# Optimization experiments

Hardware: AMD Instinct MI355X
Metric: run time of the kernel (lower is better)

The kernel has to match this reference:

```python
import jax, jax.numpy as jnp
import numpy as np

D_MODEL = 1024
NUM_HEADS = 16
SEQ_LEN = 2048
HEAD_DIM = D_MODEL // NUM_HEADS


def _rope_thetas(seq_len, head_dim):
    # Standard RoPE angles: theta[s, j] = s * 10000^(-2j/d), j in [0, d/2)
    d_half = head_dim // 2
    pos = jnp.arange(seq_len, dtype=jnp.float32)
    freqs = 1.0 / jnp.power(10000.0, jnp.arange(0, head_dim, 2, dtype=jnp.float32) / head_dim)
    thetas = pos[:, None] * freqs[None, :]  # [S, d_half]
    return jnp.cos(thetas), jnp.sin(thetas)


def _apply_rope(x, cos, sin):
    # x: [B, H, S, D]; rotate consecutive pairs (x_{2i}, x_{2i+1}) by theta_i
    b, h, s, d = x.shape
    xp = x.reshape(b, h, s, d // 2, 2)
    x1, x2 = xp[..., 0], xp[..., 1]
    c = cos[None, None, :, :]
    sn = sin[None, None, :, :]
    o1 = x1 * c - x2 * sn
    o2 = x1 * sn + x2 * c
    return jnp.stack([o1, o2], axis=-1).reshape(b, h, s, d)


def setup_inputs() -> dict:
    key = jax.random.key(0)
    k_x, k_wqkv, k_bqkv, k_wo, k_bo = jax.random.split(key, 5)
    lim_qkv = 1.0 / np.sqrt(D_MODEL)
    x = jax.random.normal(k_x, (2, SEQ_LEN, D_MODEL), dtype=jnp.float32)
    w_qkv = jax.random.uniform(k_wqkv, (3 * D_MODEL, D_MODEL), jnp.float32, -lim_qkv, lim_qkv)
    b_qkv = jax.random.uniform(k_bqkv, (3 * D_MODEL,), jnp.float32, -lim_qkv, lim_qkv)
    w_out = jax.random.uniform(k_wo, (D_MODEL, D_MODEL), jnp.float32, -lim_qkv, lim_qkv)
    b_out = jax.random.uniform(k_bo, (D_MODEL,), jnp.float32, -lim_qkv, lim_qkv)
    return {"x": x, "w_qkv": w_qkv, "b_qkv": b_qkv, "w_out": w_out, "b_out": b_out}


def reference(x, w_qkv, b_qkv, w_out, b_out):
    B, S, D = x.shape
    H, Dh = NUM_HEADS, D // NUM_HEADS
    qkv = x @ w_qkv.T + b_qkv  # [B, S, 3D]
    q, k, v = jnp.split(qkv, 3, axis=-1)
    # [B, S, D] -> [B, H, S, Dh]
    q = q.reshape(B, S, H, Dh).transpose(0, 2, 1, 3)
    k = k.reshape(B, S, H, Dh).transpose(0, 2, 1, 3)
    v = v.reshape(B, S, H, Dh).transpose(0, 2, 1, 3)
    cos, sin = _rope_thetas(S, Dh)
    q = _apply_rope(q, cos, sin)
    k = _apply_rope(k, cos, sin)
    scores = jnp.einsum('bhqd,bhkd->bhqk', q, k) / jnp.sqrt(jnp.float32(Dh))
    causal = jnp.tril(jnp.ones((S, S), dtype=bool))
    scores = jnp.where(causal[None, None, :, :], scores, jnp.float32(-jnp.inf))
    attn = jax.nn.softmax(scores, axis=-1)
    o = jnp.einsum('bhqk,bhkd->bhqd', attn, v)  # [B, H, S, Dh]
    o = o.transpose(0, 2, 1, 3).reshape(B, S, D)
    return o @ w_out.T + b_out
```

## Files before the change

### kernel.cpp

```cpp
#include <hip/hip_runtime.h>
#include <stdint.h>

#define S_LEN 2048
#define NH 16
#define DM 1024
#define HD 64
#define NB 2
#define TOK (NB * S_LEN)

typedef __attribute__((ext_vector_type(8))) short short8v;
typedef __attribute__((ext_vector_type(4))) float f32x4;
typedef __attribute__((ext_vector_type(2))) unsigned int u32x2;
typedef unsigned short u16;
typedef unsigned int u32;

__device__ __forceinline__ float bf2f(u16 u) {
    u32 x = ((u32)u) << 16;
    return __builtin_bit_cast(float, x);
}
__device__ __forceinline__ u16 f2bf(float f) {
    u32 u = __builtin_bit_cast(u32, f);
    return (u16)((u + 0x7FFFu + ((u >> 16) & 1u)) >> 16);
}
__device__ __forceinline__ u32 cvtpk(float lo, float hi) {
    u32 r;
    asm("v_cvt_pk_bf16_f32 %0, %1, %2" : "=v"(r) : "v"(lo), "v"(hi));
    return r;
}

__device__ __forceinline__ void gld_lds16(const void* g, void* lds_base_uniform) {
    auto gp = (const __attribute__((address_space(1))) u32*)(uintptr_t)g;
    auto lp = (__attribute__((address_space(3))) u32*)(uintptr_t)(u32)(uintptr_t)lds_base_uniform;
    __builtin_amdgcn_global_load_lds(gp, lp, 16, 0, 0);
}

__global__ void detect_dtype(const u32* __restrict__ xw, int* __restrict__ flag) {
    __shared__ int cnt[4];
    const int t = threadIdx.x;
    int c = 0;
#pragma unroll
    for (int j = 0; j < 16; ++j) {
        const u32 wd = xw[(t * 16 + j) * 64];
        const u32 e = (wd >> 7) & 0xFF;
        c += (e >= 0x58 && e <= 0x98) ? 1 : 0;
    }
#pragma unroll
    for (int off = 1; off < 64; off <<= 1) c += __shfl_xor(c, off);
    if ((t & 63) == 0) cnt[t >> 6] = c;
    __syncthreads();
    if (t == 0) flag[0] = (cnt[0] + cnt[1] + cnt[2] + cnt[3] >= 2600) ? 1 : 0;
}

#define XCH (TOK * DM / 8)
#define WQCH (3 * DM * DM / 8)
#define WOCH (DM * DM / 8)
#define CONVTOT (XCH + WQCH + WOCH)
#define TABN (S_LEN * 16)
__global__ __launch_bounds__(256) void convert_all(
    const void* __restrict__ xs, const void* __restrict__ wqs, const void* __restrict__ wos,
    u16* __restrict__ xd, u16* __restrict__ wqd, u16* __restrict__ wod,
    float* __restrict__ tab, const int* __restrict__ flagp) {
    int i = blockIdx.x * 256 + threadIdx.x;
    if (i >= CONVTOT) {
        const int e = i - CONVTOT;
        const int s = e & 2047;
        const int i2 = e >> 11;
        const float fa = expf(-(float)(2 * i2) * 0.2878231366242557f);
        const float fb = expf(-(float)(2 * i2 + 1) * 0.2878231366242557f);
        float sa, ca, sb, cb;
        sincosf((float)s * fa, &sa, &ca);
        sincosf((float)s * fb, &sb, &cb);
        f32x4 tv = {ca, sa, cb, sb};
        *(f32x4*)(tab + (size_t)e * 4) = tv;
        return;
    }
    const void* src;
    u16* dst;
    if (i < XCH) {
        src = xs; dst = xd;
    } else if (i < XCH + WQCH) {
        src = wqs; dst = wqd; i -= XCH;
    } else {
        src = wos; dst = wod; i -= XCH + WQCH;
    }
    if (flagp[0]) {
        ((short8v*)dst)[i] = ((const short8v*)src)[i];
    } else {
        const f32x4 v0 = ((const f32x4*)src)[2 * i];
        const f32x4 v1 = ((const f32x4*)src)[2 * i + 1];
        short8v o;
#pragma unroll
        for (int q = 0; q < 4; ++q) o[q] = (short)f2bf(v0[q]);
#pragma unroll
        for (int q = 0; q < 4; ++q) o[4 + q] = (short)f2bf(v1[q]);
        ((short8v*)dst)[i] = o;
    }
}

template <int MODE>
__global__ __launch_bounds__(256) void gemm_k(
    const u16* __restrict__ A, const u16* __restrict__ Bt,
    const void* __restrict__ biasv, void* __restrict__ Cv,
    int M, int N, int K, const int* __restrict__ flagp, int out_flagged,
    u16* __restrict__ qws, u16* __restrict__ kws,
    u16* __restrict__ vT, const float* __restrict__ tab) {
    __shared__ __align__(16) u16 lA[3][128 * 32];
    __shared__ __align__(16) u16 lB[3][128 * 32];
    const int fl = flagp[0];
    const int fo = out_flagged ? fl : 1;

    const int tid = threadIdx.x;
    const int w = __builtin_amdgcn_readfirstlane(tid >> 6);
    const int lane = tid & 63;
    const int quad = lane >> 4;
    const int l16 = lane & 15;
    const int bm = blockIdx.y * 128;
    const int bn = (MODE == 2 ? 2048 : 0) + blockIdx.x * 128;
    const int wm = (w >> 1) * 64;
    const int wn = (w & 1) * 64;

    f32x4 acc[4][4];
#pragma unroll
    for (int i = 0; i < 4; ++i)
#pragma unroll
        for (int j = 0; j < 4; ++j) acc[i][j] = {0.f, 0.f, 0.f, 0.f};

    const int kiters = K >> 5;
#define GEMM_STAGE(kk, buf)                                                            \
    {                                                                                  \
        _Pragma("unroll") for (int c = 0; c < 2; ++c) {                                \
            const int chunk = w * 2 + c;                                               \
            const int off = chunk * 1024 + lane * 16;                                  \
            const int m_ = off >> 6;                                                   \
            const int kb_ = off & 63;                                                  \
            gld_lds16((const char*)(A + (size_t)(bm + m_) * K + (kk) * 32) + kb_,      \
                      (char*)&lA[buf][0] + chunk * 1024);                              \
            gld_lds16((const char*)(Bt + (size_t)(bn + m_) * K + (kk) * 32) + kb_,     \
                      (char*)&lB[buf][0] + chunk * 1024);                              \
        }                                                                              \
    }

    GEMM_STAGE(0, 0);
    if (kiters > 1) GEMM_STAGE(1, 1);
    int cur = 0;
    for (int kk = 0; kk < kiters; ++kk) {
        if (kk + 1 < kiters) {
            asm volatile("s_waitcnt vmcnt(4)" ::: "memory");
        } else {
            asm volatile("s_waitcnt vmcnt(0)" ::: "memory");
        }
        __builtin_amdgcn_s_barrier();
        if (kk + 2 < kiters) {
            const int nb = (cur + 2 >= 3) ? cur - 1 : cur + 2;
            GEMM_STAGE(kk + 2, nb);
        }

        short8v af[4], bf[4];
#pragma unroll
        for (int t = 0; t < 4; ++t) {
            af[t] = *(const short8v*)&lA[cur][(wm + t * 16 + l16) * 32 + quad * 8];
            bf[t] = *(const short8v*)&lB[cur][(wn + t * 16 + l16) * 32 + quad * 8];
        }
        __builtin_amdgcn_s_setprio(1);
        if constexpr (MODE == 2) {
#pragma unroll
            for (int i = 0; i < 4; ++i)
#pragma unroll
                for (int j = 0; j < 4; ++j)
                    acc[i][j] =
                        __builtin_amdgcn_mfma_f32_16x16x32_bf16(af[i], bf[j], acc[i][j], 0, 0, 0);
        } else {
#pragma unroll
            for (int i = 0; i < 4; ++i)
#pragma unroll
                for (int j = 0; j < 4; ++j)
                    acc[i][j] =
                        __builtin_amdgcn_mfma_f32_16x16x32_bf16(bf[j], af[i], acc[i][j], 0, 0, 0);
        }
        __builtin_amdgcn_s_setprio(0);
        cur = (cur == 2) ? 0 : cur + 1;
    }
#undef GEMM_STAGE

    if constexpr (MODE == 0) {
#pragma unroll
        for (int j = 0; j < 4; ++j) {
            const int n0 = bn + wn + j * 16 + quad * 4;
            float bv0, bv1, bv2, bv3;
            if (fl) {
                const u32x2 bw = *(const u32x2*)((const u16*)biasv + n0);
                bv0 = bf2f((u16)(bw.x & 0xffff));
                bv1 = bf2f((u16)(bw.x >> 16));
                bv2 = bf2f((u16)(bw.y & 0xffff));
                bv3 = bf2f((u16)(bw.y >> 16));
            } else {
                const f32x4 bw = *(const f32x4*)((const float*)biasv + n0);
                bv0 = bw[0]; bv1 = bw[1]; bv2 = bw[2]; bv3 = bw[3];
            }
#pragma unroll
            for (int i = 0; i < 4; ++i) {
                const size_t base = (size_t)(bm + wm + i * 16 + l16) * N + n0;
                const float v0 = acc[i][j][0] + bv0, v1 = acc[i][j][1] + bv1;
                const float v2 = acc[i][j][2] + bv2, v3 = acc[i][j][3] + bv3;
                if (fo) {
                    u32x2 ov;
                    ov.x = cvtpk(v0, v1);
                    ov.y = cvtpk(v2, v3);
                    *(u32x2*)((u16*)Cv + base) = ov;
                } else {
                    f32x4 ov = {v0, v1, v2, v3};
                    *(f32x4*)((float*)Cv + base) = ov;
                }
            }
        }
    } else if constexpr (MODE == 2) {
#pragma unroll
        for (int j = 0; j < 4; ++j) {
            const int n = bn + wn + j * 16 + l16;
            const float bv = fl ? bf2f(((const u16*)biasv)[n]) : ((const float*)biasv)[n];
            const int vcol = n - 2048;
            const int hh = vcol >> 6, d = vcol & 63;
#pragma unroll
            for (int i = 0; i < 4; ++i) {
                const int m0 = bm + wm + i * 16 + quad * 4;
                const int bb = m0 >> 11, s0 = m0 & 2047;
                u32x2 ov;
                ov.x = cvtpk(acc[i][j][0] + bv, acc[i][j][1] + bv);
                ov.y = cvtpk(acc[i][j][2] + bv, acc[i][j][3] + bv);
                *(u32x2*)(vT + ((size_t)((bb * NH + hh) * HD + d)) * S_LEN + s0) = ov;
            }
        }
    } else {
        const bool isq = (blockIdx.x < 8);
        u16* outp = isq ? qws : kws;
#pragma unroll
        for (int j = 0; j < 4; ++j) {
            const int n0 = bn + wn + j * 16 + quad * 4;
            float bv0, bv1, bv2, bv3;
            if (fl) {
                const u32x2 bw = *(const u32x2*)((const u16*)biasv + n0);
                bv0 = bf2f((u16)(bw.x & 0xffff));
                bv1 = bf2f((u16)(bw.x >> 16));
                bv2 = bf2f((u16)(bw.y & 0xffff));
                bv3 = bf2f((u16)(bw.y >> 16));
            } else {
                const f32x4 bw = *(const f32x4*)((const float*)biasv + n0);
                bv0 = bw[0]; bv1 = bw[1]; bv2 = bw[2]; bv3 = bw[3];
            }
            const int nc = n0 & 1023;
            const int hh = nc >> 6;
            const int d0 = nc & 63;
            const int i2u = d0 >> 2;
#pragma unroll
            for (int i = 0; i < 4; ++i) {
                const int m = bm + wm + i * 16 + l16;
                const int bb = m >> 11, s = m & 2047;
                const f32x4 cs4 = *(const f32x4*)(tab + ((size_t)i2u * S_LEN + s) * 4);
                const float v0 = acc[i][j][0] + bv0, v1 = acc[i][j][1] + bv1;
                const float v2 = acc[i][j][2] + bv2, v3 = acc[i][j][3] + bv3;
                const float o0 = v0 * cs4[0] - v1 * cs4[1];
                const float o1 = v0 * cs4[1] + v1 * cs4[0];
                const float o2 = v2 * cs4[2] - v3 * cs4[3];
                const float o3 = v2 * cs4[3] + v3 * cs4[2];
                u32x2 ov;
                ov.x = cvtpk(o0, o1);
                ov.y = cvtpk(o2, o3);
                *(u32x2*)(outp + ((size_t)((bb * NH + hh) * S_LEN + s)) * HD + d0) = ov;
            }
        }
    }
}

__global__ __launch_bounds__(256, 4) void attn_kernel(
    const u16* __restrict__ qws, const u16* __restrict__ kws,
    const u16* __restrict__ vT, u16* __restrict__ ows) {
    __shared__ __align__(16) u16 kl[2][64 * 64];
    __shared__ __align__(16) u16 vl[64 * 64];
    __shared__ __align__(16) u32 pl32[4][16 * 36];
    const int t = threadIdx.x;
    const int w = __builtin_amdgcn_readfirstlane(t >> 6);
    const int lane = t & 63;
    const int quad = lane >> 4;
    const int l16 = lane & 15;

    const int id = blockIdx.x;
    const int g = id & 31;
    const int qb = 31 - (id >> 5);
    const int h = g & 15, b = g >> 4;
    const int q0 = qb * 64 + w * 16;

    const size_t bh = (size_t)(b * NH + h);
    const u16* qbp = qws + bh * (size_t)S_LEN * HD;
    const u16* kb = kws + bh * (size_t)S_LEN * HD;
    const u16* vb = vT + bh * (size_t)HD * S_LEN;

    const int r0 = lane >> 3;
    const int srcc = (lane & 7) ^ r0;
    const int xorb = (l16 & 7) << 4;

    short8v qf[2];
#pragma unroll
    for (int hf = 0; hf < 2; ++hf)
        qf[hf] = *(const short8v*)(qbp + (size_t)(q0 + l16) * HD + hf * 32 + quad * 8);

    f32x4 oaccT[4];
#pragma unroll
    for (int d = 0; d < 4; ++d) oaccT[d] = {0.f, 0.f, 0.f, 0.f};
    float mrow = -__builtin_inff();
    float lrow = 0.f;

#pragma unroll
    for (int s = 0; s < 2; ++s) {
        const int row = w * 8 + s * 32 + r0;
        gld_lds16(kb + (size_t)row * HD + srcc * 8, (char*)&kl[0][0] + w * 1024 + s * 4096);
    }

    int cur = 0;
    for (int kt = 0; kt <= qb; ++kt) {
        __syncthreads();
#pragma unroll
        for (int s = 0; s < 2; ++s) {
            const int row = w * 8 + s * 32 + r0;
            gld_lds16(vb + (size_t)row * S_LEN + kt * 64 + srcc * 8,
                      (char*)&vl[0] + w * 1024 + s * 4096);
        }
        if (kt < qb) {
#pragma unroll
            for (int s = 0; s < 2; ++s) {
                const int row = w * 8 + s * 32 + r0;
                gld_lds16(kb + (size_t)((kt + 1) * 64 + row) * HD + srcc * 8,
                          (char*)&kl[cur ^ 1][0] + w * 1024 + s * 4096);
            }
        }
        const char* Kb = (const char*)&kl[cur][0];

        f32x4 s4[4];
        __builtin_amdgcn_s_setprio(1);
#pragma unroll
        for (int sub = 0; sub < 4; ++sub) {
            const int lin = (sub * 16 + l16) * 128 + quad * 16;
            const short8v k0 = *(const short8v*)(Kb + (lin ^ xorb));
            const short8v k1 = *(const short8v*)(Kb + ((lin + 64) ^ xorb));
            f32x4 a = {0.f, 0.f, 0.f, 0.f};
            a = __builtin_amdgcn_mfma_f32_16x16x32_bf16(k0, qf[0], a, 0, 0, 0);
            a = __builtin_amdgcn_mfma_f32_16x16x32_bf16(k1, qf[1], a, 0, 0, 0);
            s4[sub] = a;
        }
        __builtin_amdgcn_s_setprio(0);
        float sv[16];
#pragma unroll
        for (int sub = 0; sub < 4; ++sub)
#pragma unroll
            for (int r = 0; r < 4; ++r) sv[sub * 4 + r] = s4[sub][r] * 0.125f;
        if (kt == qb) {
            const int qloc = w * 16 + l16;
#pragma unroll
            for (int sub = 0; sub < 4; ++sub)
#pragma unroll
                for (int r = 0; r < 4; ++r)
                    if (sub * 16 + quad * 4 + r > qloc) sv[sub * 4 + r] = -__builtin_inff();
        }
        float a0 = fmaxf(sv[0], sv[1]), a1 = fmaxf(sv[2], sv[3]);
        float a2 = fmaxf(sv[4], sv[5]), a3 = fmaxf(sv[6], sv[7]);
        float a4 = fmaxf(sv[8], sv[9]), a5 = fmaxf(sv[10], sv[11]);
        float a6 = fmaxf(sv[12], sv[13]), a7 = fmaxf(sv[14], sv[15]);
        a0 = fmaxf(a0, a1); a2 = fmaxf(a2, a3);
        a4 = fmaxf(a4, a5); a6 = fmaxf(a6, a7);
        a0 = fmaxf(a0, a2); a4 = fmaxf(a4, a6);
        float mx = fmaxf(a0, a4);
        mx = fmaxf(mx, __shfl_xor(mx, 16));
        mx = fmaxf(mx, __shfl_xor(mx, 32));
        const float mnew = fmaxf(mrow, mx);
        const float alpha = __expf(mrow - mnew);
        mrow = mnew;
        float p[16];
#pragma unroll
        for (int i = 0; i < 16; ++i) p[i] = __expf(sv[i] - mnew);
        float b0 = p[0] + p[1], b1 = p[2] + p[3], b2 = p[4] + p[5], b3 = p[6] + p[7];
        float b4 = p[8] + p[9], b5 = p[10] + p[11], b6 = p[12] + p[13], b7 = p[14] + p[15];
        b0 += b1; b2 += b3; b4 += b5; b6 += b7;
        b0 += b2; b4 += b6;
        float ps = b0 + b4;
        ps += __shfl_xor(ps, 16);
        ps += __shfl_xor(ps, 32);
        lrow = lrow * alpha + ps;
#pragma unroll
        for (int d = 0; d < 4; ++d) oaccT[d] *= alpha;
        u32* prow = &pl32[w][l16 * 36];
#pragma unroll
        for (int sub = 0; sub < 4; ++sub) {
            u32x2 pw;
            pw.x = cvtpk(p[sub * 4 + 0], p[sub * 4 + 1]);
            pw.y = cvtpk(p[sub * 4 + 2], p[sub * 4 + 3]);
            *(u32x2*)&prow[sub * 8 + quad * 2] = pw;
        }
        asm volatile("s_waitcnt lgkmcnt(0)" ::: "memory");
        if (kt < qb) {
            asm volatile("s_waitcnt vmcnt(2)" ::: "memory");
        } else {
            asm volatile("s_waitcnt vmcnt(0)" ::: "memory");
        }
        __builtin_amdgcn_s_barrier();
        asm volatile("" ::: "memory");
        __builtin_amdgcn_s_setprio(1);
#pragma unroll
        for (int c2 = 0; c2 < 2; ++c2) {
            const short8v pf = *(const short8v*)&pl32[w][l16 * 36 + c2 * 16 + quad * 4];
#pragma unroll
            for (int d = 0; d < 4; ++d) {
                const int lin = (d * 16 + l16) * 128 + c2 * 64 + quad * 16;
                const short8v vfd = *(const short8v*)((const char*)&vl[0] + (lin ^ xorb));
                oaccT[d] = __builtin_amdgcn_mfma_f32_16x16x32_bf16(vfd, pf, oaccT[d], 0, 0, 0);
            }
        }
        __builtin_amdgcn_s_setprio(0);
        cur ^= 1;
    }

    const float inv = 1.0f / lrow;
    const size_t rowbase = ((size_t)(b * S_LEN + q0 + l16)) * DM + h * HD;
#pragma unroll
    for (int df = 0; df < 4; ++df) {
        const int d0 = df * 16 + quad * 4;
        u32x2 ov;
        ov.x = cvtpk(oaccT[df][0] * inv, oaccT[df][1] * inv);
        ov.y = cvtpk(oaccT[df][2] * inv, oaccT[df][3] * inv);
        *(u32x2*)(ows + rowbase + d0) = ov;
    }
}

extern "C" void kernel_launch(void* const* d_in, const int* in_sizes, int n_in,
                              void* d_out, int out_size, void* d_ws, size_t ws_size,
                              hipStream_t stream) {
    const void* x = d_in[0];
    const void* w_qkv = d_in[1];
    const void* b_qkv = d_in[2];
    const void* w_out = d_in[3];
    const void* b_out = d_in[4];

    int* flag = (int*)d_ws;
    u16* xb = (u16*)d_ws + 8;
    u16* wqkvb = xb + (size_t)TOK * DM;
    u16* woutb = wqkvb + (size_t)3 * DM * DM;
    u16* qws = woutb + (size_t)DM * DM;
    u16* kws = qws + (size_t)NB * NH * S_LEN * HD;
    u16* vT = kws + (size_t)NB * NH * S_LEN * HD;
    u16* ows = vT + (size_t)NB * NH * HD * S_LEN;
    float* tab = (float*)(ows + (size_t)TOK * DM);

    detect_dtype<<<1, 256, 0, stream>>>((const u32*)x, flag);
    convert_all<<<(CONVTOT + TABN) / 256, 256, 0, stream>>>(
        x, w_qkv, w_out, xb, wqkvb, woutb, tab, flag);

    gemm_k<1><<<dim3(16, TOK / 128), 256, 0, stream>>>(
        xb, wqkvb, b_qkv, nullptr, TOK, 3 * DM, DM, flag, 0, qws, kws, nullptr, tab);
    gemm_k<2><<<dim3(8, TOK / 128), 256, 0, stream>>>(
        xb, wqkvb, b_qkv, nullptr, TOK, 3 * DM, DM, flag, 0, nullptr, nullptr, vT, nullptr);
    attn_kernel<<<dim3(32 * 32), 256, 0, stream>>>(qws, kws, vT, ows);
    gemm_k<0><<<dim3(DM / 128, TOK / 128), 256, 0, stream>>>(
        ows, woutb, b_out, d_out, TOK, DM, DM, flag, 1, nullptr, nullptr, nullptr, nullptr);
}
```

Baseline: 206.8 us.

## Triple-buffer K and double-buffer V in attention to drop one barrier per tile

The attention loop now keeps K in a three-slot LDS ring and V in a two-slot ring. V for the next tile and K two tiles ahead are prefetched right after a single barrier at the top of each iteration. This replaces the old pattern of one __syncthreads plus a second barrier before the PV MFMA, so the V load has a full iteration to overlap with compute. LDS per block grows and launch bounds drop from 4 to 3 blocks per CU, so occupancy may fall.

```diff
diff --git a/kernel.cpp b/kernel.cpp
--- a/kernel.cpp
+++ b/kernel.cpp
@@ -271,11 +271,11 @@
     }
 }
 
-__global__ __launch_bounds__(256, 4) void attn_kernel(
+__global__ __launch_bounds__(256, 3) void attn_kernel(
     const u16* __restrict__ qws, const u16* __restrict__ kws,
     const u16* __restrict__ vT, u16* __restrict__ ows) {
-    __shared__ __align__(16) u16 kl[2][64 * 64];
-    __shared__ __align__(16) u16 vl[64 * 64];
+    __shared__ __align__(16) u16 kl[3][64 * 64];
+    __shared__ __align__(16) u16 vl[2][64 * 64];
     __shared__ __align__(16) u32 pl32[4][16 * 36];
     const int t = threadIdx.x;
     const int w = __builtin_amdgcn_readfirstlane(t >> 6);
@@ -309,30 +309,43 @@
     float mrow = -__builtin_inff();
     float lrow = 0.f;
 
-#pragma unroll
-    for (int s = 0; s < 2; ++s) {
-        const int row = w * 8 + s * 32 + r0;
-        gld_lds16(kb + (size_t)row * HD + srcc * 8, (char*)&kl[0][0] + w * 1024 + s * 4096);
-    }
-
-    int cur = 0;
+#define STAGE_K(kt, buf)                                                            \
+    {                                                                               \
+        _Pragma("unroll") for (int s = 0; s < 2; ++s) {                             \
+            const int row = w * 8 + s * 32 + r0;                                    \
+            gld_lds16(kb + (size_t)((kt) * 64 + row) * HD + srcc * 8,               \
+                      (char*)&kl[buf][0] + w * 1024 + s * 4096);                    \
+        }                                                                           \
+    }
+#define STAGE_V(kt, buf)                                                            \
+    {                                                                               \
+        _Pragma("unroll") for (int s = 0; s < 2; ++s) {                             \
+            const int row = w * 8 + s * 32 + r0;                                    \
+            gld_lds16(vb + (size_t)row * S_LEN + (kt) * 64 + srcc * 8,              \
+                      (char*)&vl[buf][0] + w * 1024 + s * 4096);                    \
+        }                                                                           \
+    }
+
+    STAGE_K(0, 0);
+    STAGE_V(0, 0);
+    if (qb >= 1) STAGE_K(1, 1);
+
+    int ck = 0;
     for (int kt = 0; kt <= qb; ++kt) {
-        __syncthreads();
-#pragma unroll
-        for (int s = 0; s < 2; ++s) {
-            const int row = w * 8 + s * 32 + r0;
-            gld_lds16(vb + (size_t)row * S_LEN + kt * 64 + srcc * 8,
-                      (char*)&vl[0] + w * 1024 + s * 4096);
-        }
         if (kt < qb) {
-#pragma unroll
-            for (int s = 0; s < 2; ++s) {
-                const int row = w * 8 + s * 32 + r0;
-                gld_lds16(kb + (size_t)((kt + 1) * 64 + row) * HD + srcc * 8,
-                          (char*)&kl[cur ^ 1][0] + w * 1024 + s * 4096);
-            }
-        }
-        const char* Kb = (const char*)&kl[cur][0];
+            asm volatile("s_waitcnt vmcnt(2)" ::: "memory");
+        } else {
+            asm volatile("s_waitcnt vmcnt(0)" ::: "memory");
+        }
+        __builtin_amdgcn_s_barrier();
+        asm volatile("" ::: "memory");
+        if (kt < qb) STAGE_V(kt + 1, (kt + 1) & 1);
+        if (kt + 2 <= qb) {
+            const int kn = (ck + 2 >= 3) ? ck - 1 : ck + 2;
+            STAGE_K(kt + 2, kn);
+        }
+        const char* Kb = (const char*)&kl[ck][0];
+        const char* Vb = (const char*)&vl[kt & 1][0];
 
         f32x4 s4[4];
         __builtin_amdgcn_s_setprio(1);
@@ -395,13 +408,7 @@
             *(u32x2*)&prow[sub * 8 + quad * 2] = pw;
         }
         asm volatile("s_waitcnt lgkmcnt(0)" ::: "memory");
-        if (kt < qb) {
-            asm volatile("s_waitcnt vmcnt(2)" ::: "memory");
-        } else {
-            asm volatile("s_waitcnt vmcnt(0)" ::: "memory");
-        }
-        __builtin_amdgcn_s_barrier();
-        asm volatile("" ::: "memory");
+        __builtin_amdgcn_sched_barrier(0);
         __builtin_amdgcn_s_setprio(1);
 #pragma unroll
         for (int c2 = 0; c2 < 2; ++c2) {
@@ -409,13 +416,15 @@
 #pragma unroll
             for (int d = 0; d < 4; ++d) {
                 const int lin = (d * 16 + l16) * 128 + c2 * 64 + quad * 16;
-                const short8v vfd = *(const short8v*)((const char*)&vl[0] + (lin ^ xorb));
+                const short8v vfd = *(const short8v*)(Vb + (lin ^ xorb));
                 oaccT[d] = __builtin_amdgcn_mfma_f32_16x16x32_bf16(vfd, pf, oaccT[d], 0, 0, 0);
             }
         }
         __builtin_amdgcn_s_setprio(0);
-        cur ^= 1;
-    }
+        ck = (ck == 2) ? 0 : ck + 1;
+    }
+#undef STAGE_K
+#undef STAGE_V
 
     const float inv = 1.0f / lrow;
     const size_t rowbase = ((size_t)(b * S_LEN + q0 + l16)) * DM + h * HD;
```

Result: no change. 209.8 us (+1.5%).
